# Kernel tuning notes

Hardware: AMD Instinct MI355X
Metric: run time of the kernel (lower is better)

The kernel has to match this reference:

```python
import jax, jax.numpy as jnp
import numpy as np

B, S, H, I = 4, 2048, 2048, 8192
LN_EPS = 1e-6  # DeepSpeed inference layer-norm epsilon


def setup_inputs() -> dict:
    key = jax.random.key(0)
    ks = jax.random.split(key, 10)
    return {
        "input": jax.random.normal(ks[0], (B, S, H), dtype=jnp.float32),
        "residual": jax.random.normal(ks[1], (B, S, H), dtype=jnp.float32),
        "residual_norm": jax.random.normal(ks[2], (B, S, H), dtype=jnp.float32),
        "bias": jax.random.normal(ks[3], (H,), dtype=jnp.float32) * 0.02,
        "gamma": jnp.ones((H,), dtype=jnp.float32) + jax.random.normal(ks[4], (H,), dtype=jnp.float32) * 0.02,
        "beta": jax.random.normal(ks[5], (H,), dtype=jnp.float32) * 0.02,
        "inter_w": jax.random.normal(ks[6], (H, I), dtype=jnp.float32) * 0.02,
        "inter_b": jax.random.normal(ks[7], (I,), dtype=jnp.float32) * 0.02,
        "output_w": jax.random.normal(ks[8], (I, H), dtype=jnp.float32) * 0.02,
        "output_b": jax.random.normal(ks[9], (H,), dtype=jnp.float32) * 0.02,
    }


def reference(input, residual, residual_norm, bias, gamma, beta,
              inter_w, inter_b, output_w, output_b):
    # --- mlp_gemm_func (pre-LN path, attn_nw is not None) ---
    # Fused: residual_add = attention_output + attention_bias + residual
    residual_add = input + residual + bias                    # [B,S,H]
    # LayerNorm over hidden dim
    mu = jnp.mean(residual_add, axis=-1, keepdims=True)
    var = jnp.mean(jnp.square(residual_add - mu), axis=-1, keepdims=True)
    ln = (residual_add - mu) * jax.lax.rsqrt(var + LN_EPS) * gamma + beta
    # GEMM + bias + GeLU, then second GEMM
    h = jax.nn.gelu(jnp.einsum("bsh,hi->bsi", ln, inter_w) + inter_b,
                    approximate=False)                        # [B,S,I]
    out = jnp.einsum("bsi,ih->bsh", h, output_w)              # [B,S,H]
    # --- residual_add_func (pre-LN, mlp_after_attn): mlp_out + residual_add + final_bias ---
    return out + residual_add + output_b
```

## Files before the change

kernel.cpp:

```cpp
#include <hip/hip_runtime.h>

typedef __attribute__((ext_vector_type(8))) __bf16 bf16x8;
typedef __attribute__((ext_vector_type(4))) float f32x4;

#define AS1(p) ((const __attribute__((address_space(1))) void*)(uintptr_t)(p))
#define AS3(p) ((__attribute__((address_space(3))) void*)(uint32_t)(uintptr_t)(p))
#define GLD16(gp, lp) __builtin_amdgcn_global_load_lds(AS1(gp), AS3(lp), 16, 0, 0)

static constexpr int Bb = 4, Ss = 2048, Hh = 2048, Ih = 8192;
static constexpr int Mm = Bb * Ss;

__device__ __forceinline__ float gelu_exact(float x) {
    return 0.5f * x * (1.0f + erff(x * 0.70710678118654752440f));
}

__global__ __launch_bounds__(256) void transpose_cvt(const float* __restrict__ src,
                                                     __bf16* __restrict__ dst,
                                                     int R, int C) {
    __shared__ float tile[32][33];
    const int tx = threadIdx.x, ty = threadIdx.y;
    const int cB = blockIdx.x * 32, rB = blockIdx.y * 32;
#pragma unroll
    for (int i = 0; i < 4; ++i)
        tile[ty + i * 8][tx] = src[(size_t)(rB + ty + i * 8) * C + cB + tx];
    __syncthreads();
#pragma unroll
    for (int i = 0; i < 4; ++i)
        dst[(size_t)(cB + ty + i * 8) * R + rB + tx] = (__bf16)tile[tx][ty + i * 8];
}

__global__ __launch_bounds__(256) void fused_ln(const float* __restrict__ input,
                                                const float* __restrict__ residual,
                                                const float* __restrict__ bias,
                                                const float* __restrict__ gamma,
                                                const float* __restrict__ beta,
                                                __bf16* __restrict__ lnb,
                                                __bf16* __restrict__ rab) {
    const int row = blockIdx.x;
    const int tid = threadIdx.x;
    const size_t base = (size_t)row * Hh;
    const int e = tid * 8;

    float4 x0 = *(const float4*)(input + base + e);
    float4 x1 = *(const float4*)(input + base + e + 4);
    float4 r0 = *(const float4*)(residual + base + e);
    float4 r1 = *(const float4*)(residual + base + e + 4);
    float4 b0 = *(const float4*)(bias + e);
    float4 b1 = *(const float4*)(bias + e + 4);

    float s[8];
    s[0] = x0.x + r0.x + b0.x; s[1] = x0.y + r0.y + b0.y;
    s[2] = x0.z + r0.z + b0.z; s[3] = x0.w + r0.w + b0.w;
    s[4] = x1.x + r1.x + b1.x; s[5] = x1.y + r1.y + b1.y;
    s[6] = x1.z + r1.z + b1.z; s[7] = x1.w + r1.w + b1.w;

    float sum = 0.f, sq = 0.f;
#pragma unroll
    for (int j = 0; j < 8; ++j) { sum += s[j]; sq += s[j] * s[j]; }
#pragma unroll
    for (int o = 32; o > 0; o >>= 1) {
        sum += __shfl_xor(sum, o);
        sq  += __shfl_xor(sq, o);
    }
    __shared__ float red[8];
    const int wv = tid >> 6, ln_ = tid & 63;
    if (ln_ == 0) { red[wv] = sum; red[4 + wv] = sq; }
    __syncthreads();
    sum = red[0] + red[1] + red[2] + red[3];
    sq  = red[4] + red[5] + red[6] + red[7];

    const float mu   = sum * (1.0f / Hh);
    const float var  = sq * (1.0f / Hh) - mu * mu;
    const float rstd = rsqrtf(var + 1e-6f);

    float4 g0 = *(const float4*)(gamma + e);
    float4 g1 = *(const float4*)(gamma + e + 4);
    float4 t0 = *(const float4*)(beta + e);
    float4 t1 = *(const float4*)(beta + e + 4);
    float g[8] = {g0.x, g0.y, g0.z, g0.w, g1.x, g1.y, g1.z, g1.w};
    float t[8] = {t0.x, t0.y, t0.z, t0.w, t1.x, t1.y, t1.z, t1.w};

    bf16x8 lv, rv;
#pragma unroll
    for (int j = 0; j < 8; ++j) {
        rv[j] = (__bf16)s[j];
        lv[j] = (__bf16)((s[j] - mu) * rstd * g[j] + t[j]);
    }
    *(bf16x8*)(lnb + base + e) = lv;
    *(bf16x8*)(rab + base + e) = rv;
}


__device__ __forceinline__ void ldA4(const char* p0, const char* p1, const int mhOff,
                                     bf16x8 (&af)[4][2]) {
#pragma unroll
    for (int m = 0; m < 4; ++m) {
        af[m][0] = *(const bf16x8*)(p0 + mhOff + m * 2048);
        af[m][1] = *(const bf16x8*)(p1 + mhOff + m * 2048);
    }
}
__device__ __forceinline__ void ldB2(const char* p0, const char* p1, const int nhOff,
                                     bf16x8 (&bf)[2][2]) {
#pragma unroll
    for (int n = 0; n < 2; ++n) {
        bf[n][0] = *(const bf16x8*)(p0 + nhOff + n * 2048);
        bf[n][1] = *(const bf16x8*)(p1 + nhOff + n * 2048);
    }
}
template <int MH, int NH>
__device__ __forceinline__ void mfmaQ(const bf16x8 (&af)[4][2], const bf16x8 (&bf)[2][2],
                                      f32x4 (&acc)[8][4]) {
#pragma unroll
    for (int m = 0; m < 4; ++m)
#pragma unroll
        for (int n = 0; n < 2; ++n)
#pragma unroll
            for (int ks = 0; ks < 2; ++ks)
                acc[MH * 4 + m][NH * 2 + n] = __builtin_amdgcn_mfma_f32_16x16x32_bf16(
                    af[m][ks], bf[n][ks], acc[MH * 4 + m][NH * 2 + n], 0, 0, 0);
}
__device__ __forceinline__ void stage2(const __bf16* src, __bf16* dst, const size_t row64) {
    GLD16(src, dst);
    GLD16(src + row64, dst + 4096);
}

#define PHASE_MID                                         \
    __builtin_amdgcn_s_barrier();                         \
    asm volatile("s_waitcnt lgkmcnt(0)" ::: "memory");    \
    __builtin_amdgcn_sched_barrier(0);                    \
    __builtin_amdgcn_s_setprio(1)
#define PHASE_END                                         \
    __builtin_amdgcn_s_setprio(0);                        \
    __builtin_amdgcn_s_barrier()

template <int MODE>
__global__ __launch_bounds__(512, 2) void gemm256(const __bf16* __restrict__ A,
                                                  const __bf16* __restrict__ Bt,
                                                  const float* __restrict__ bias,
                                                  const __bf16* __restrict__ rab,
                                                  __bf16* __restrict__ outH,
                                                  float* __restrict__ outF,
                                                  int M, int N, int K) {
    __shared__ __align__(128) __bf16 lds[2 * 4 * 128 * 64];

    const int tid = threadIdx.x;
    const int nbx = N >> 8;
    const int nwg = gridDim.x;
    const int cpx = nwg >> 3;
    const int bid = blockIdx.x;
    const int swz = (bid & 7) * cpx + (bid >> 3);
    const int by = swz / nbx, bx = swz - by * nbx;
    const int mBase = by << 8, nBase = bx << 8;

    const int wave = tid >> 6, lane = tid & 63;
    const int wr = wave >> 2, wc = wave & 3;

    const int NT = K >> 6;
    const int NI = NT >> 1;

    char* ldsc = (char*)lds;
    const int laneCol0 = (((lane >> 4) << 4)) ^ ((lane & 7) << 4);
    const int laneCol1 = laneCol0 ^ 64;
    const int aLaneR = (lane & 15) << 7;
    const int bLaneR = (((wc & 1) << 6) + (lane & 15)) << 7;
    const char* pA[2][2] = {
        {ldsc + (0 * 4 + wr) * 16384 + aLaneR + laneCol0,
         ldsc + (0 * 4 + wr) * 16384 + aLaneR + laneCol1},
        {ldsc + (1 * 4 + wr) * 16384 + aLaneR + laneCol0,
         ldsc + (1 * 4 + wr) * 16384 + aLaneR + laneCol1}};
    const char* pB[2][2] = {
        {ldsc + (0 * 4 + 2 + (wc >> 1)) * 16384 + bLaneR + laneCol0,
         ldsc + (0 * 4 + 2 + (wc >> 1)) * 16384 + bLaneR + laneCol1},
        {ldsc + (1 * 4 + 2 + (wc >> 1)) * 16384 + bLaneR + laneCol0,
         ldsc + (1 * 4 + 2 + (wc >> 1)) * 16384 + bLaneR + laneCol1}};

    const int srow = tid >> 3;
    const int scol = ((tid & 7) ^ (srow & 7)) << 3;
    const __bf16* aSt = A + (size_t)(mBase + srow) * K + scol;
    const __bf16* bSt = Bt + (size_t)(nBase + srow) * K + scol;
    __bf16* lw = lds + tid * 8;
    const size_t row64 = (size_t)64 * K;
    const size_t row128 = (size_t)128 * K;

#define STA(buf, h, t) stage2(aSt + (h) * row128 + (size_t)(t) * 64, lw + ((buf) * 4 + (h)) * 8192, row64)
#define STB(buf, h, t) stage2(bSt + (h) * row128 + (size_t)(t) * 64, lw + ((buf) * 4 + 2 + (h)) * 8192, row64)

    f32x4 acc[8][4] = {};
    bf16x8 af[4][2], b0[2][2], b1[2][2];

    STA(0, 0, 0); STA(0, 1, 0); STB(0, 0, 0); STB(0, 1, 0);
    STB(1, 0, 1); STB(1, 1, 1);
    asm volatile("s_waitcnt vmcnt(4)" ::: "memory");
    __builtin_amdgcn_s_barrier();

    for (int i = 0; i < NI; ++i) {
        const int t0 = 2 * i, t1 = 2 * i + 1;
        const bool pf0 = (t0 + 2 < NT);
        const bool pf1 = (t1 + 2 < NT);

        ldA4(pA[0][0], pA[0][1], 0, af);
        ldB2(pB[0][0], pB[0][1], 0, b0);
        STA(1, 0, t1);
        PHASE_MID; mfmaQ<0, 0>(af, b0, acc); PHASE_END;

        ldB2(pB[0][0], pB[0][1], 4096, b1);
        STA(1, 1, t1);
        PHASE_MID; mfmaQ<0, 1>(af, b1, acc); PHASE_END;

        ldA4(pA[0][0], pA[0][1], 8192, af);
        if (pf0) STB(0, 0, t0 + 2);
        PHASE_MID; mfmaQ<1, 1>(af, b1, acc); PHASE_END;

        if (pf0) STB(0, 1, t0 + 2);
        PHASE_MID; mfmaQ<1, 0>(af, b0, acc);
        __builtin_amdgcn_s_setprio(0);
        if (pf0) { asm volatile("s_waitcnt vmcnt(4)" ::: "memory"); }
        else     { asm volatile("s_waitcnt vmcnt(0)" ::: "memory"); }
        __builtin_amdgcn_s_barrier();

        ldA4(pA[1][0], pA[1][1], 0, af);
        ldB2(pB[1][0], pB[1][1], 0, b0);
        if (pf0) STA(0, 0, t0 + 2);
        PHASE_MID; mfmaQ<0, 0>(af, b0, acc); PHASE_END;

        ldB2(pB[1][0], pB[1][1], 4096, b1);
        if (pf0) STA(0, 1, t0 + 2);
        PHASE_MID; mfmaQ<0, 1>(af, b1, acc); PHASE_END;

        ldA4(pA[1][0], pA[1][1], 8192, af);
        if (pf1) STB(1, 0, t1 + 2);
        PHASE_MID; mfmaQ<1, 1>(af, b1, acc); PHASE_END;

        if (pf1) STB(1, 1, t1 + 2);
        PHASE_MID; mfmaQ<1, 0>(af, b0, acc);
        __builtin_amdgcn_s_setprio(0);
        if (pf1) { asm volatile("s_waitcnt vmcnt(4)" ::: "memory"); }
        __builtin_amdgcn_s_barrier();
    }

    const int r0 = mBase + wr * 128 + ((lane >> 4) << 2);
    const int c0 = nBase + wc * 64 + (lane & 15);
    float bb[4];
#pragma unroll
    for (int nf = 0; nf < 4; ++nf) bb[nf] = bias[c0 + nf * 16];
#pragma unroll
    for (int mf = 0; mf < 8; ++mf) {
        const int row = r0 + mf * 16;
#pragma unroll
        for (int nf = 0; nf < 4; ++nf) {
            const int col = c0 + nf * 16;
#pragma unroll
            for (int j = 0; j < 4; ++j) {
                const size_t idx = (size_t)(row + j) * N + col;
                const float v = acc[mf][nf][j] + bb[nf];
                if (MODE == 0) {
                    outH[idx] = (__bf16)gelu_exact(v);
                } else {
                    outF[idx] = v + (float)rab[idx];
                }
            }
        }
    }
#undef STA
#undef STB
}

extern "C" void kernel_launch(void* const* d_in, const int* in_sizes, int n_in,
                              void* d_out, int out_size, void* d_ws, size_t ws_size,
                              hipStream_t stream) {
    const float* input    = (const float*)d_in[0];
    const float* residual = (const float*)d_in[1];
    const float* bias     = (const float*)d_in[3];
    const float* gamma    = (const float*)d_in[4];
    const float* beta     = (const float*)d_in[5];
    const float* inter_w  = (const float*)d_in[6];
    const float* inter_b  = (const float*)d_in[7];
    const float* output_w = (const float*)d_in[8];
    const float* output_b = (const float*)d_in[9];
    float* out = (float*)d_out;

    __bf16* w1t  = (__bf16*)d_ws;
    __bf16* w2t  = w1t + (size_t)Ih * Hh;
    __bf16* lnb  = w2t + (size_t)Hh * Ih;
    __bf16* rab  = lnb + (size_t)Mm * Hh;
    __bf16* hbuf = rab + (size_t)Mm * Hh;

    transpose_cvt<<<dim3(Ih / 32, Hh / 32), dim3(32, 8), 0, stream>>>(inter_w, w1t, Hh, Ih);
    transpose_cvt<<<dim3(Hh / 32, Ih / 32), dim3(32, 8), 0, stream>>>(output_w, w2t, Ih, Hh);

    fused_ln<<<Mm, 256, 0, stream>>>(input, residual, bias, gamma, beta, lnb, rab);

    gemm256<0><<<dim3((Mm / 256) * (Ih / 256)), 512, 0, stream>>>(
        lnb, w1t, inter_b, nullptr, hbuf, nullptr, Mm, Ih, Hh);

    gemm256<1><<<dim3((Mm / 256) * (Hh / 256)), 512, 0, stream>>>(
        hbuf, w2t, output_b, rab, nullptr, out, Mm, Hh, Ih);
}
```

Baseline: 608.8 us.

## Prefetch both A fragment halves up front and use partial lgkmcnt waits in GEMM loop

Restructures the inner K-loop of the 256x256 bf16 MFMA GEMM. Each tile now issues all LDS reads for both A halves and the first B half at the start, into separate register sets. Each MFMA quadrant then waits only with partial lgkmcnt counts, so LDS reads overlap the preceding MFMAs instead of draining with lgkmcnt(0) every phase. The quadrant order changes to 00,10,11,01 to match what has arrived, and the sched_barrier is replaced by compiler memory fences around barriers. The extra A fragment registers raise VGPR pressure under the 512-thread, 2-block launch bounds.

```diff
diff --git a/kernel.cpp b/kernel.cpp
--- a/kernel.cpp
+++ b/kernel.cpp
@@ -91,6 +91,9 @@
 }
 
 
+#define CFENCE asm volatile("" ::: "memory")
+#define BAR()  do { CFENCE; __builtin_amdgcn_s_barrier(); CFENCE; } while (0)
+
 __device__ __forceinline__ void ldA4(const char* p0, const char* p1, const int mhOff,
                                      bf16x8 (&af)[4][2]) {
 #pragma unroll
@@ -108,7 +111,7 @@
     }
 }
 template <int MH, int NH>
-__device__ __forceinline__ void mfmaQ(const bf16x8 (&af)[4][2], const bf16x8 (&bf)[2][2],
+__device__ __forceinline__ void mfmaQ(const bf16x8 (&a)[4][2], const bf16x8 (&b)[2][2],
                                       f32x4 (&acc)[8][4]) {
 #pragma unroll
     for (int m = 0; m < 4; ++m)
@@ -117,21 +120,12 @@
 #pragma unroll
             for (int ks = 0; ks < 2; ++ks)
                 acc[MH * 4 + m][NH * 2 + n] = __builtin_amdgcn_mfma_f32_16x16x32_bf16(
-                    af[m][ks], bf[n][ks], acc[MH * 4 + m][NH * 2 + n], 0, 0, 0);
+                    a[m][ks], b[n][ks], acc[MH * 4 + m][NH * 2 + n], 0, 0, 0);
 }
 __device__ __forceinline__ void stage2(const __bf16* src, __bf16* dst, const size_t row64) {
     GLD16(src, dst);
     GLD16(src + row64, dst + 4096);
 }
-
-#define PHASE_MID                                         \
-    __builtin_amdgcn_s_barrier();                         \
-    asm volatile("s_waitcnt lgkmcnt(0)" ::: "memory");    \
-    __builtin_amdgcn_sched_barrier(0);                    \
-    __builtin_amdgcn_s_setprio(1)
-#define PHASE_END                                         \
-    __builtin_amdgcn_s_setprio(0);                        \
-    __builtin_amdgcn_s_barrier()
 
 template <int MODE>
 __global__ __launch_bounds__(512, 2) void gemm256(const __bf16* __restrict__ A,
@@ -186,57 +180,68 @@
 #define STB(buf, h, t) stage2(bSt + (h) * row128 + (size_t)(t) * 64, lw + ((buf) * 4 + 2 + (h)) * 8192, row64)
 
     f32x4 acc[8][4] = {};
-    bf16x8 af[4][2], b0[2][2], b1[2][2];
+    bf16x8 a0v[4][2], a1v[4][2], b0v[2][2], b1v[2][2];
 
     STA(0, 0, 0); STA(0, 1, 0); STB(0, 0, 0); STB(0, 1, 0);
     STB(1, 0, 1); STB(1, 1, 1);
     asm volatile("s_waitcnt vmcnt(4)" ::: "memory");
-    __builtin_amdgcn_s_barrier();
+    BAR();
+
+#define TILE(bi, S1, S2, S3, S4, BOUND)                                        \
+    ldA4(pA[bi][0], pA[bi][1], 0, a0v);                                        \
+    ldB2(pB[bi][0], pB[bi][1], 0, b0v);                                        \
+    ldA4(pA[bi][0], pA[bi][1], 8192, a1v);                                     \
+    S1;                                                                        \
+    BAR();                                                                     \
+    asm volatile("s_waitcnt lgkmcnt(8)" ::: "memory");                         \
+    __builtin_amdgcn_s_setprio(1);                                             \
+    mfmaQ<0, 0>(a0v, b0v, acc);                                                \
+    __builtin_amdgcn_s_setprio(0);                                             \
+    BAR();                                                                     \
+    ldB2(pB[bi][0], pB[bi][1], 4096, b1v);                                     \
+    S2;                                                                        \
+    BAR();                                                                     \
+    asm volatile("s_waitcnt lgkmcnt(4)" ::: "memory");                         \
+    __builtin_amdgcn_s_setprio(1);                                             \
+    mfmaQ<1, 0>(a1v, b0v, acc);                                                \
+    __builtin_amdgcn_s_setprio(0);                                             \
+    BAR();                                                                     \
+    S3;                                                                        \
+    BAR();                                                                     \
+    asm volatile("s_waitcnt lgkmcnt(0)" ::: "memory");                         \
+    __builtin_amdgcn_s_setprio(1);                                             \
+    mfmaQ<1, 1>(a1v, b1v, acc);                                                \
+    __builtin_amdgcn_s_setprio(0);                                             \
+    BAR();                                                                     \
+    S4;                                                                        \
+    BAR();                                                                     \
+    __builtin_amdgcn_s_setprio(1);                                             \
+    mfmaQ<0, 1>(a0v, b1v, acc);                                                \
+    __builtin_amdgcn_s_setprio(0);                                             \
+    BOUND;                                                                     \
+    BAR();
 
     for (int i = 0; i < NI; ++i) {
         const int t0 = 2 * i, t1 = 2 * i + 1;
         const bool pf0 = (t0 + 2 < NT);
         const bool pf1 = (t1 + 2 < NT);
 
-        ldA4(pA[0][0], pA[0][1], 0, af);
-        ldB2(pB[0][0], pB[0][1], 0, b0);
-        STA(1, 0, t1);
-        PHASE_MID; mfmaQ<0, 0>(af, b0, acc); PHASE_END;
-
-        ldB2(pB[0][0], pB[0][1], 4096, b1);
-        STA(1, 1, t1);
-        PHASE_MID; mfmaQ<0, 1>(af, b1, acc); PHASE_END;
-
-        ldA4(pA[0][0], pA[0][1], 8192, af);
-        if (pf0) STB(0, 0, t0 + 2);
-        PHASE_MID; mfmaQ<1, 1>(af, b1, acc); PHASE_END;
-
-        if (pf0) STB(0, 1, t0 + 2);
-        PHASE_MID; mfmaQ<1, 0>(af, b0, acc);
-        __builtin_amdgcn_s_setprio(0);
-        if (pf0) { asm volatile("s_waitcnt vmcnt(4)" ::: "memory"); }
-        else     { asm volatile("s_waitcnt vmcnt(0)" ::: "memory"); }
-        __builtin_amdgcn_s_barrier();
-
-        ldA4(pA[1][0], pA[1][1], 0, af);
-        ldB2(pB[1][0], pB[1][1], 0, b0);
-        if (pf0) STA(0, 0, t0 + 2);
-        PHASE_MID; mfmaQ<0, 0>(af, b0, acc); PHASE_END;
-
-        ldB2(pB[1][0], pB[1][1], 4096, b1);
-        if (pf0) STA(0, 1, t0 + 2);
-        PHASE_MID; mfmaQ<0, 1>(af, b1, acc); PHASE_END;
-
-        ldA4(pA[1][0], pA[1][1], 8192, af);
-        if (pf1) STB(1, 0, t1 + 2);
-        PHASE_MID; mfmaQ<1, 1>(af, b1, acc); PHASE_END;
-
-        if (pf1) STB(1, 1, t1 + 2);
-        PHASE_MID; mfmaQ<1, 0>(af, b0, acc);
-        __builtin_amdgcn_s_setprio(0);
-        if (pf1) { asm volatile("s_waitcnt vmcnt(4)" ::: "memory"); }
-        __builtin_amdgcn_s_barrier();
-    }
+        TILE(0,
+             STA(1, 0, t1),
+             STA(1, 1, t1),
+             if (pf0) STB(0, 0, t0 + 2),
+             if (pf0) STB(0, 1, t0 + 2),
+             if (pf0) { asm volatile("s_waitcnt vmcnt(4)" ::: "memory"); }
+             else     { asm volatile("s_waitcnt vmcnt(0)" ::: "memory"); })
+
+        TILE(1,
+             if (pf0) STA(0, 0, t0 + 2),
+             if (pf0) STA(0, 1, t0 + 2),
+             if (pf1) STB(1, 0, t1 + 2),
+             if (pf1) STB(1, 1, t1 + 2),
+             if (pf1) { asm volatile("s_waitcnt vmcnt(4)" ::: "memory"); })
+    }
+#undef TILE
 
     const int r0 = mBase + wr * 128 + ((lane >> 4) << 2);
     const int c0 = nBase + wc * 64 + (lane & 15);
```

After: 692.7 us. 13.8% more time.
